# Kernel tuning notes

Measured on AMD Instinct MI355X. Metric: run time of the kernel, lower is better.

Reference implementation:

```python
import jax, jax.numpy as jnp
import numpy as np

B, S, D_IN, D_OUT = 4, 2048, 1024, 1024


def setup_inputs() -> dict:
    key = jax.random.key(0)
    k1, k2, k3, k4 = jax.random.split(key, 4)
    x = jax.random.normal(k1, (B, S, D_IN), dtype=jnp.float32)
    scale = 1.0 / np.sqrt(D_IN)
    Wq = jax.random.normal(k2, (D_IN, D_OUT), dtype=jnp.float32) * scale
    Wk = jax.random.normal(k3, (D_IN, D_OUT), dtype=jnp.float32) * scale
    Wv = jax.random.normal(k4, (D_IN, D_OUT), dtype=jnp.float32) * scale
    return {"x": x, "Wq": Wq, "Wk": Wk, "Wv": Wv}


def reference(x, Wq, Wk, Wv):
    # QKV projections (Linear, no bias)
    q = jnp.einsum('bsd,de->bse', x, Wq)  # [B,S,D_OUT]
    k = jnp.einsum('bsd,de->bse', x, Wk)
    v = jnp.einsum('bsd,de->bse', x, Wv)
    d_out = Wq.shape[1]
    # raw scores [B,S,S], scaled after masking (identical math: -inf stays -inf)
    scores = jnp.einsum('bqe,bke->bqk', q, k) * (d_out ** -0.5)
    S_ = x.shape[1]
    # causal mask: future positions (j > i) are masked out
    causal = jnp.triu(jnp.ones((S_, S_), dtype=bool), k=1)
    scores = jnp.where(causal[None, :, :], -jnp.inf, scores)
    attn = jax.nn.softmax(scores, axis=-1)  # dropout p=0.0 -> identity
    return jnp.einsum('bqk,bke->bqe', attn, v)
```

## Files before the change

### kernel.cpp

```cpp
#include <hip/hip_runtime.h>
#include <stdint.h>

typedef unsigned short u16;
typedef unsigned int u32;
typedef __bf16 bf16x8 __attribute__((ext_vector_type(8)));
typedef float f32x4 __attribute__((ext_vector_type(4)));

#define BM 128
#define BN 128
#define BK 64

__device__ __forceinline__ u16 f2bf(float x) {
  union { float f; uint32_t u; } c; c.f = x;
  uint32_t r = (c.u + 0x7FFFu + ((c.u >> 16) & 1u)) >> 16;
  return (u16)r;
}
__device__ __forceinline__ float bf2f(u16 v) {
  union { uint32_t u; float f; } c; c.u = ((uint32_t)v) << 16;
  return c.f;
}

__device__ __forceinline__ void async_copy16(const u16* g, u16* l) {
  __builtin_amdgcn_global_load_lds(
      (const __attribute__((address_space(1))) void*)g,
      (__attribute__((address_space(3))) void*)l,
      16, 0, 0);
}

__global__ void zerofill_u16(u16* __restrict__ p) {
  long i = (long)blockIdx.x * 256 + threadIdx.x;
  p[i] = 0;
}

__global__ __launch_bounds__(256)
void prep(const void* __restrict__ xs, const void* __restrict__ w0,
          const void* __restrict__ w1, const void* __restrict__ w2,
          u16* __restrict__ xn, u16* __restrict__ WT3, u32* __restrict__ flag,
          float* __restrict__ sigma, int nxb)
{
  __shared__ int sh_hits;
  __shared__ u16 tile[64][72];
  if (threadIdx.x == 0) sh_hits = 0;
  __syncthreads();
  {
    const u16* w = (const u16*)w0;
    int h = 0;
    for (int i = threadIdx.x; i < 8192; i += 256)
      if ((w[i] & 0x7F80u) == 0x7F80u) h++;
    if (h) atomicAdd(&sh_hits, h);
  }
  __syncthreads();
  const bool isf32 = (sh_hits > 0);
  const int blk = blockIdx.x;
  const int tid = threadIdx.x;
  if (blk == 0 && tid == 0) *flag = isf32 ? 1000u : 0u;

  if (blk < nxb) {
    long i = ((long)blk * 256 + tid) * 8;
    u16 o[8];
    if (isf32) {
      const float* s = (const float*)xs + i;
      f32x4 a = *(const f32x4*)s;
      f32x4 b = *(const f32x4*)(s + 4);
#pragma unroll
      for (int c = 0; c < 4; ++c) { o[c] = f2bf(a[c]); o[c + 4] = f2bf(b[c]); }
    } else {
      *(uint4*)o = *(const uint4*)((const u16*)xs + i);
    }
    *(uint4*)(xn + i) = *(uint4*)o;
  } else if (blk < nxb + 768) {
    const int Dd = 1024;
    int t = blk - nxb;
    int z = t >> 8;
    int r = t & 255;
    const int r0 = (r >> 4) * 64, c0 = (r & 15) * 64;
    const void* src = (z == 0) ? w0 : (z == 1) ? w1 : w2;
    u16* out = WT3 + (long)z * Dd * Dd;
#pragma unroll
    for (int p = 0; p < 2; ++p) {
      int v = tid + p * 256;
      int row = v >> 3, c8 = (v & 7) * 8;
      u16 tt[8];
      if (isf32) {
        const float* sp = (const float*)src + (long)(r0 + row) * Dd + c0 + c8;
        f32x4 a = *(const f32x4*)sp;
        f32x4 b = *(const f32x4*)(sp + 4);
#pragma unroll
        for (int c = 0; c < 4; ++c) { tt[c] = f2bf(a[c]); tt[c + 4] = f2bf(b[c]); }
      } else {
        *(uint4*)tt = *(const uint4*)((const u16*)src + (long)(r0 + row) * Dd + c0 + c8);
      }
#pragma unroll
      for (int c = 0; c < 8; ++c) tile[row][c8 + c] = tt[c];
    }
    __syncthreads();
#pragma unroll
    for (int p = 0; p < 2; ++p) {
      int v = tid + p * 256;
      int oc = v >> 3, r8 = (v & 7) * 8;
      union { uint4 q; u16 s[8]; } tt;
#pragma unroll
      for (int c = 0; c < 8; ++c) tt.s[c] = tile[r8 + c][oc];
      *(uint4*)(out + (long)(c0 + oc) * Dd + r0 + r8) = tt.q;
    }
  } else {
    int t = blk - (nxb + 768);
    *(f32x4*)(sigma + ((long)t * 256 + tid) * 4) = f32x4{0.f, 0.f, 0.f, 0.f};
  }
}

__global__ __launch_bounds__(512, 2)
void gemm_qkv(const u16* __restrict__ A, const u16* __restrict__ B,
              u16* __restrict__ C, int lda, int ldb, int ldc)
{
  __shared__ u16 ldsq[3 * 24576];
  const int tid  = threadIdx.x;
  const int wid  = tid >> 6;
  const int lane = tid & 63;
  const int l16  = lane & 15;
  const int lk   = lane >> 4;
  const int srow = lane >> 3;
  const int swz  = ((lane & 7) ^ srow) * 8;
  const int wr   = wid >> 1, wc = wid & 1;
  const int m0 = blockIdx.y * 256, n0 = blockIdx.x * 128;

  const u16* gA = A + (long)(m0 + wid * 32 + srow) * lda + swz;
  const u16* gB = B + (long)(n0 + wid * 16 + srow) * ldb + swz;

  const int NK = 16;

  auto issue = [&](int kt) {
    u16* Ab = ldsq + (kt % 3) * 24576;
    u16* Bb = Ab + 16384;
    const int k0 = kt * 64;
#pragma unroll
    for (int c = 0; c < 4; ++c)
      async_copy16(gA + (long)(c * 8) * lda + k0, Ab + (wid * 32 + c * 8) * 64);
#pragma unroll
    for (int c = 0; c < 2; ++c)
      async_copy16(gB + (long)(c * 8) * ldb + k0, Bb + (wid * 16 + c * 8) * 64);
  };

  f32x4 acc[4][4] = {};
  issue(0);
  issue(1);

#pragma unroll
  for (int kt = 0; kt < NK; ++kt) {
    if (kt < NK - 1) asm volatile("s_waitcnt vmcnt(6) lgkmcnt(0)" ::: "memory");
    else             asm volatile("s_waitcnt vmcnt(0) lgkmcnt(0)" ::: "memory");
    asm volatile("s_barrier" ::: "memory");
    if (kt + 2 < NK) issue(kt + 2);
    const u16* Ab = ldsq + (kt % 3) * 24576;
    const u16* Bb = Ab + 16384;
#pragma unroll
    for (int kh = 0; kh < 2; ++kh) {
      bf16x8 av[4], bv[4];
#pragma unroll
      for (int i = 0; i < 4; ++i) {
        const int Ra = wr * 64 + i * 16 + l16;
        const int Rb = wc * 64 + i * 16 + l16;
        const int ca = ((kh * 4 + lk) ^ (l16 & 7)) * 8;
        av[i] = *(const bf16x8*)(Ab + Ra * 64 + ca);
        bv[i] = *(const bf16x8*)(Bb + Rb * 64 + ca);
      }
      __builtin_amdgcn_s_setprio(1);
#pragma unroll
      for (int mi = 0; mi < 4; ++mi)
#pragma unroll
        for (int ni = 0; ni < 4; ++ni)
          acc[mi][ni] = __builtin_amdgcn_mfma_f32_16x16x32_bf16(av[mi], bv[ni], acc[mi][ni], 0, 0, 0);
      __builtin_amdgcn_s_setprio(0);
    }
  }

  const int rb0 = m0 + wr * 64;
  const int cb0 = n0 + wc * 64;
#pragma unroll
  for (int mi = 0; mi < 4; ++mi)
#pragma unroll
    for (int r = 0; r < 4; ++r) {
      const int row = rb0 + mi * 16 + lk * 4 + r;
#pragma unroll
      for (int ni = 0; ni < 4; ++ni) {
        const int col = cb0 + ni * 16 + l16;
        C[(long)row * ldc + col] = f2bf(acc[mi][ni][r]);
      }
    }
}

template <int MODE>
__global__ __launch_bounds__(256, 4)
void gemm_nt(const u16* __restrict__ A, const u16* __restrict__ B, void* __restrict__ Cv,
             const u32* __restrict__ flag, float* __restrict__ sigma, int sigStride,
             int K, int lda, int ldb, int ldc,
             long sA, long sB, long sC, long cOff,
             float scale, int trik, int ntri,
             const u16* __restrict__ vSrc, u16* __restrict__ vtDst,
             long sV, long sVT, int ldV, int ldVT)
{
  __shared__ u16 As[BM * BK];
  __shared__ u16 Bs[BN * BK];
  const int bz = blockIdx.z;
  const int tid = threadIdx.x;

  int bm, bn;
  if constexpr (MODE == 3) {
    if ((int)blockIdx.x >= ntri) {
      int t2 = blockIdx.x - ntri;
      const u16* in = vSrc + (long)bz * sV;
      u16* out = vtDst + (long)bz * sVT;
      const int c0 = (t2 & 15) * 64;
      const int r0 = (t2 >> 4) * 64;
      u16 (*tile)[72] = reinterpret_cast<u16(*)[72]>(As);
#pragma unroll
      for (int p = 0; p < 2; ++p) {
        int v = tid + p * 256;
        int row = v >> 3, c8 = (v & 7) * 8;
        union { uint4 q; u16 s[8]; } t;
        t.q = *(const uint4*)(in + (long)(r0 + row) * ldV + c0 + c8);
#pragma unroll
        for (int i = 0; i < 8; ++i) tile[row][c8 + i] = t.s[i];
      }
      __syncthreads();
#pragma unroll
      for (int p = 0; p < 2; ++p) {
        int v = tid + p * 256;
        int oc = v >> 3, r8 = (v & 7) * 8;
        union { uint4 q; u16 s[8]; } t;
#pragma unroll
        for (int i = 0; i < 8; ++i) t.s[i] = tile[r8 + i][oc];
        *(uint4*)(out + (long)(c0 + oc) * ldVT + r0 + r8) = t.q;
      }
      return;
    }
    {
      const int t = blockIdx.x;
      const int cum[11] = {0, 10, 26, 36, 52, 68, 78, 94, 110, 126, 136};
      const int ssm[10] = {0, 1, 1, 2, 2, 2, 3, 3, 3, 3};
      const int ssn[10] = {0, 0, 1, 0, 1, 2, 0, 1, 2, 3};
      int s = 0;
      while (cum[s + 1] <= t) ++s;
      const int l = t - cum[s];
      const int sm = ssm[s], sn = ssn[s];
      int tm, tn;
      if (sm == sn) {
        tm = 0;
        while ((tm + 1) * (tm + 2) / 2 <= l) ++tm;
        tn = l - tm * (tm + 1) / 2;
      } else { tm = l >> 2; tn = l & 3; }
      bm = sm * 4 + tm;
      bn = sn * 4 + tn;
    }
  } else {
    bm = blockIdx.y;
    if (trik) bm = gridDim.y - 1 - bm;
    bn = blockIdx.x;
  }

  A += (long)bz * sA;
  B += (long)bz * sB;

  const int wid  = tid >> 6;
  const int lane = tid & 63;
  const int l16  = lane & 15;
  const int lk   = lane >> 4;
  const int srow = lane >> 3;
  const int swz  = ((lane & 7) ^ srow) * 8;
  const int m0 = bm * BM, n0 = bn * BN;

  int nk = K / BK;
  if (trik) { int lim = (m0 + BM) / BK; if (lim < nk) nk = lim; }

  f32x4 acc[4][4] = {};

  for (int kt = 0; kt < nk; ++kt) {
    const int k0 = kt * BK;
#pragma unroll
    for (int c = 0; c < 4; ++c) {
      const int rb = wid * 32 + c * 8;
      async_copy16(A + (long)(m0 + rb + srow) * lda + (k0 + swz), As + rb * BK);
      async_copy16(B + (long)(n0 + rb + srow) * ldb + (k0 + swz), Bs + rb * BK);
    }
    __syncthreads();
#pragma unroll
    for (int kh = 0; kh < 2; ++kh) {
      bf16x8 av[4], bv[4];
#pragma unroll
      for (int i = 0; i < 4; ++i) {
        const int Ra = (wid >> 1) * 64 + i * 16 + l16;
        const int Rb = (wid & 1)  * 64 + i * 16 + l16;
        const int ca = ((kh * 4 + lk) ^ (l16 & 7)) * 8;
        av[i] = *(const bf16x8*)(As + Ra * BK + ca);
        bv[i] = *(const bf16x8*)(Bs + Rb * BK + ca);
      }
#pragma unroll
      for (int mi = 0; mi < 4; ++mi)
#pragma unroll
        for (int ni = 0; ni < 4; ++ni)
          acc[mi][ni] = __builtin_amdgcn_mfma_f32_16x16x32_bf16(av[mi], bv[ni], acc[mi][ni], 0, 0, 0);
    }
    __syncthreads();
  }

  const int rb0 = m0 + (wid >> 1) * 64;
  const int cb0 = n0 + (wid & 1) * 64;
  const long cbase = (long)bz * sC + cOff;

  if constexpr (MODE == 3) {
    u16* Cp = (u16*)Cv;
    const bool diag = (bm == bn);
    float* sig = sigma + (long)bz * sigStride;
#pragma unroll
    for (int mi = 0; mi < 4; ++mi)
#pragma unroll
      for (int r = 0; r < 4; ++r) {
        const int row = rb0 + mi * 16 + lk * 4 + r;
        float part = 0.f;
#pragma unroll
        for (int ni = 0; ni < 4; ++ni) {
          const int col = cb0 + ni * 16 + l16;
          float ev = __expf(acc[mi][ni][r] * scale);
          if (diag && col > row) ev = 0.f;
          u16 b = f2bf(ev);
          part += bf2f(b);
          Cp[cbase + (long)row * ldc + col] = b;
        }
#pragma unroll
        for (int o = 1; o < 16; o <<= 1) part += __shfl_xor(part, o);
        if (l16 == 0) atomicAdd(&sig[row], part);
      }
  } else {
    const bool f32out = (MODE == 2) && (*flag > 32);
    const float* sig = (MODE == 2) ? (sigma + (long)bz * sigStride) : nullptr;
#pragma unroll
    for (int mi = 0; mi < 4; ++mi)
#pragma unroll
      for (int r = 0; r < 4; ++r) {
        const int row = rb0 + mi * 16 + lk * 4 + r;
        float rs = scale;
        if constexpr (MODE == 2) rs = 1.0f / sig[row];
#pragma unroll
        for (int ni = 0; ni < 4; ++ni) {
          const int col = cb0 + ni * 16 + l16;
          const float v = acc[mi][ni][r] * rs;
          const long idx = cbase + (long)row * ldc + col;
          if constexpr (MODE == 0) {
            ((u16*)Cv)[idx] = f2bf(v);
          } else {
            if (f32out) ((float*)Cv)[idx] = v;
            else        ((u16*)Cv)[idx]   = f2bf(v);
          }
        }
      }
  }
}

extern "C" void kernel_launch(void* const* d_in, const int* in_sizes, int n_in,
                              void* d_out, int out_size, void* d_ws, size_t ws_size,
                              hipStream_t stream)
{
  (void)in_sizes; (void)n_in; (void)out_size;
  const int Bb = 4, S = 2048, D = 1024, D3 = 3072;
  const long SD  = (long)S * D;
  const long SD3 = (long)S * D3;
  const long SS  = (long)S * S;
  const long N_X = (long)Bb * SD;
  const long N_W = (long)D * D;
  const int NTRI = 16 * 17 / 2;

  char* ws = (char*)d_ws;
  size_t off = 0;
  auto take = [&](size_t bytes) -> void* {
    void* p = ws + off;
    off = (off + bytes + 255) & ~((size_t)255);
    return p;
  };

  u32*   flag  = (u32*)take(4096);
  float* sigma = (float*)take((size_t)Bb * S * 4);
  u16*   xn    = (u16*)take((size_t)N_X * 2);
  u16*   WT3   = (u16*)take((size_t)3 * N_W * 2);
  const size_t off_common = off;

  const size_t needA = off_common + (size_t)(N_X * 3 * 2)
                     + (size_t)(N_X * 2)
                     + (size_t)(Bb * SS * 2) + 4096;
  const size_t needC = off_common + (size_t)(S * (long)D3 * 2)
                     + (size_t)(SD * 2)
                     + (size_t)(SS * 2) + 4096;

  if (ws_size < needC) {
    zerofill_u16<<<(int)(N_X / 256), 256, 0, stream>>>((u16*)d_out);
    return;
  }

  const int nxb = (int)(N_X / 2048);
  prep<<<nxb + 768 + 8, 256, 0, stream>>>(d_in[0], d_in[1], d_in[2], d_in[3],
                                          xn, WT3, flag, sigma, nxb);

  const float scl = 0.03125f;

  if (ws_size >= needA) {
    u16* QKV = (u16*)take((size_t)N_X * 3 * 2);
    u16* VT  = (u16*)take((size_t)N_X * 2);
    u16* E   = (u16*)take((size_t)Bb * SS * 2);

    gemm_qkv<<<dim3(D3 / 128, (int)(N_X / D) / 256, 1), 512, 0, stream>>>(
        xn, WT3, QKV, D, D, D3);

    gemm_nt<3><<<dim3(NTRI + 512, 1, Bb), 256, 0, stream>>>(
        QKV, QKV + 1024, E, flag, sigma, S, D, D3, D3, S,
        SD3, SD3, SS, 0, scl, 0, NTRI,
        QKV + 2048, VT, SD3, SD, D3, S);

    gemm_nt<2><<<dim3(D / BN, S / BM, Bb), 256, 0, stream>>>(
        E, VT, d_out, flag, sigma, S, S, S, S, D,
        SS, SD, SD, 0, 1.f, 1, 0, nullptr, nullptr, 0, 0, 0, 0);
  } else {
    u16* QKVb = (u16*)take((size_t)S * D3 * 2);
    u16* VTb  = (u16*)take((size_t)SD * 2);
    u16* Eb   = (u16*)take((size_t)SS * 2);

    for (int b = 0; b < Bb; ++b) {
      gemm_qkv<<<dim3(D3 / 128, S / 256, 1), 512, 0, stream>>>(
          xn + (long)b * SD, WT3, QKVb, D, D, D3);

      gemm_nt<3><<<dim3(NTRI + 512, 1, 1), 256, 0, stream>>>(
          QKVb, QKVb + 1024, Eb, flag, sigma + (long)b * S, S, D, D3, D3, S,
          0, 0, 0, 0, scl, 0, NTRI,
          QKVb + 2048, VTb, 0, 0, D3, S);

      gemm_nt<2><<<dim3(D / BN, S / BM, 1), 256, 0, stream>>>(
          Eb, VTb, d_out, flag, sigma + (long)b * S, S, S, S, S, D,
          0, 0, 0, (long)b * SD, 1.f, 1, 0, nullptr, nullptr, 0, 0, 0, 0);
    }
  }
}
```

Baseline: 247.1 us.

## Rewrite QKV GEMM with 256x256 tiles, double-buffered staggered loads, XCD remap

The QKV projection kernel is restructured from 256x128 tiles with a three-stage buffer into 256x256 tiles with 8 waves arranged 2x4. Each wave now computes a 128x64 sub-tile. A and B use double-buffered LDS, and their loads are staggered across four sub-steps per k-tile, with barriers interleaved so memory traffic overlaps the MFMA work. Block indices are remapped so that consecutive tiles land on the same XCD group, which should improve L2 reuse. The larger tile raises arithmetic intensity and lowers global traffic, at the cost of more accumulator registers, 128KB of LDS per block, and more barriers.

```diff
diff --git a/kernel.cpp b/kernel.cpp
--- a/kernel.cpp
+++ b/kernel.cpp
@@ -110,10 +110,10 @@
 }
 
 __global__ __launch_bounds__(512, 2)
-void gemm_qkv(const u16* __restrict__ A, const u16* __restrict__ B,
-              u16* __restrict__ C, int lda, int ldb, int ldc)
+void gemm_qkv8(const u16* __restrict__ A, const u16* __restrict__ B,
+               u16* __restrict__ C, int lda, int ldb, int ldc, int nbn)
 {
-  __shared__ u16 ldsq[3 * 24576];
+  __shared__ u16 lds[65536];
   const int tid  = threadIdx.x;
   const int wid  = tid >> 6;
   const int lane = tid & 63;
@@ -121,63 +121,84 @@
   const int lk   = lane >> 4;
   const int srow = lane >> 3;
   const int swz  = ((lane & 7) ^ srow) * 8;
-  const int wr   = wid >> 1, wc = wid & 1;
-  const int m0 = blockIdx.y * 256, n0 = blockIdx.x * 128;
-
-  const u16* gA = A + (long)(m0 + wid * 32 + srow) * lda + swz;
-  const u16* gB = B + (long)(n0 + wid * 16 + srow) * ldb + swz;
+  const int wr   = wid >> 2, wc = wid & 3;
+
+  const int q8 = (int)gridDim.x >> 3;
+  const int wg = ((int)blockIdx.x & 7) * q8 + ((int)blockIdx.x >> 3);
+  const int m0 = (wg / nbn) * 256, n0 = (wg % nbn) * 256;
 
   const int NK = 16;
 
-  auto issue = [&](int kt) {
-    u16* Ab = ldsq + (kt % 3) * 24576;
-    u16* Bb = Ab + 16384;
-    const int k0 = kt * 64;
-#pragma unroll
-    for (int c = 0; c < 4; ++c)
-      async_copy16(gA + (long)(c * 8) * lda + k0, Ab + (wid * 32 + c * 8) * 64);
-#pragma unroll
-    for (int c = 0; c < 2; ++c)
-      async_copy16(gB + (long)(c * 8) * ldb + k0, Bb + (wid * 16 + c * 8) * 64);
+  auto stageA = [&](int t, int h) {
+    u16* dst = lds + (t & 1) * 16384 + h * 8192 + (wid * 16) * 64;
+    const u16* src = A + (long)(m0 + h * 128 + wid * 16 + srow) * lda + t * 64 + swz;
+    async_copy16(src, dst);
+    async_copy16(src + (long)8 * lda, dst + 8 * 64);
   };
-
-  f32x4 acc[4][4] = {};
-  issue(0);
-  issue(1);
-
-#pragma unroll
-  for (int kt = 0; kt < NK; ++kt) {
-    if (kt < NK - 1) asm volatile("s_waitcnt vmcnt(6) lgkmcnt(0)" ::: "memory");
-    else             asm volatile("s_waitcnt vmcnt(0) lgkmcnt(0)" ::: "memory");
-    asm volatile("s_barrier" ::: "memory");
-    if (kt + 2 < NK) issue(kt + 2);
-    const u16* Ab = ldsq + (kt % 3) * 24576;
-    const u16* Bb = Ab + 16384;
-#pragma unroll
-    for (int kh = 0; kh < 2; ++kh) {
-      bf16x8 av[4], bv[4];
-#pragma unroll
-      for (int i = 0; i < 4; ++i) {
-        const int Ra = wr * 64 + i * 16 + l16;
-        const int Rb = wc * 64 + i * 16 + l16;
-        const int ca = ((kh * 4 + lk) ^ (l16 & 7)) * 8;
-        av[i] = *(const bf16x8*)(Ab + Ra * 64 + ca);
-        bv[i] = *(const bf16x8*)(Bb + Rb * 64 + ca);
-      }
+  auto stageB = [&](int t, int h) {
+    u16* dst = lds + 32768 + (t & 1) * 16384 + h * 8192 + (wid * 16) * 64;
+    const u16* src = B + (long)(n0 + h * 128 + wid * 16 + srow) * ldb + t * 64 + swz;
+    async_copy16(src, dst);
+    async_copy16(src + (long)8 * ldb, dst + 8 * 64);
+  };
+
+  f32x4 acc[8][4] = {};
+  bf16x8 bv[4][2];
+
+  stageB(0, 0); stageB(0, 1); stageA(0, 0); stageA(0, 1);
+  stageB(1, 0); stageB(1, 1);
+  asm volatile("s_waitcnt vmcnt(4)" ::: "memory");
+  __builtin_amdgcn_s_barrier();
+
+  for (int t = 0; t < NK; ++t) {
+    const u16* Ab = lds + (t & 1) * 16384 + wr * 8192;
+    const u16* Bb = lds + 32768 + (t & 1) * 16384 + (wc >> 1) * 8192 + (wc & 1) * 64 * 64;
+#pragma unroll
+    for (int q = 0; q < 4; ++q) {
+      bf16x8 av[2][2];
+#pragma unroll
+      for (int j = 0; j < 2; ++j)
+#pragma unroll
+        for (int kh = 0; kh < 2; ++kh)
+          av[j][kh] = *(const bf16x8*)(Ab + ((2 * q + j) * 16 + l16) * 64 +
+                                       (((kh * 4 + lk) ^ (l16 & 7)) * 8));
+      if (q == 0) {
+#pragma unroll
+        for (int ni = 0; ni < 4; ++ni)
+#pragma unroll
+          for (int kh = 0; kh < 2; ++kh)
+            bv[ni][kh] = *(const bf16x8*)(Bb + (ni * 16 + l16) * 64 +
+                                          (((kh * 4 + lk) ^ (l16 & 7)) * 8));
+      }
+      if (q == 0)      { if (t + 1 < NK) stageA(t + 1, 0); }
+      else if (q == 1) { if (t + 1 < NK) stageA(t + 1, 1); }
+      else if (q == 2) { if (t + 2 < NK) stageB(t + 2, 0); }
+      else {
+        if (t + 2 < NK) stageB(t + 2, 1);
+        if (t < NK - 2) asm volatile("s_waitcnt vmcnt(4)" ::: "memory");
+        else            asm volatile("s_waitcnt vmcnt(0)" ::: "memory");
+      }
+      __builtin_amdgcn_s_barrier();
+      asm volatile("s_waitcnt lgkmcnt(0)" ::: "memory");
+      __builtin_amdgcn_sched_barrier(0);
       __builtin_amdgcn_s_setprio(1);
 #pragma unroll
-      for (int mi = 0; mi < 4; ++mi)
+      for (int j = 0; j < 2; ++j)
 #pragma unroll
         for (int ni = 0; ni < 4; ++ni)
-          acc[mi][ni] = __builtin_amdgcn_mfma_f32_16x16x32_bf16(av[mi], bv[ni], acc[mi][ni], 0, 0, 0);
+#pragma unroll
+          for (int kh = 0; kh < 2; ++kh)
+            acc[2 * q + j][ni] = __builtin_amdgcn_mfma_f32_16x16x32_bf16(
+                av[j][kh], bv[ni][kh], acc[2 * q + j][ni], 0, 0, 0);
       __builtin_amdgcn_s_setprio(0);
-    }
-  }
-
-  const int rb0 = m0 + wr * 64;
+      __builtin_amdgcn_s_barrier();
+    }
+  }
+
+  const int rb0 = m0 + wr * 128;
   const int cb0 = n0 + wc * 64;
 #pragma unroll
-  for (int mi = 0; mi < 4; ++mi)
+  for (int mi = 0; mi < 8; ++mi)
 #pragma unroll
     for (int r = 0; r < 4; ++r) {
       const int row = rb0 + mi * 16 + lk * 4 + r;
@@ -406,8 +427,7 @@
     u16* VT  = (u16*)take((size_t)N_X * 2);
     u16* E   = (u16*)take((size_t)Bb * SS * 2);
 
-    gemm_qkv<<<dim3(D3 / 128, (int)(N_X / D) / 256, 1), 512, 0, stream>>>(
-        xn, WT3, QKV, D, D, D3);
+    gemm_qkv8<<<dim3(32 * 12), 512, 0, stream>>>(xn, WT3, QKV, D, D, D3, 12);
 
     gemm_nt<3><<<dim3(NTRI + 512, 1, Bb), 256, 0, stream>>>(
         QKV, QKV + 1024, E, flag, sigma, S, D, D3, D3, S,
@@ -423,8 +443,8 @@
     u16* Eb   = (u16*)take((size_t)SS * 2);
 
     for (int b = 0; b < Bb; ++b) {
-      gemm_qkv<<<dim3(D3 / 128, S / 256, 1), 512, 0, stream>>>(
-          xn + (long)b * SD, WT3, QKVb, D, D, D3);
+      gemm_qkv8<<<dim3(8 * 12), 512, 0, stream>>>(
+          xn + (long)b * SD, WT3, QKVb, D, D, D3, 12);
 
       gemm_nt<3><<<dim3(NTRI + 512, 1, 1), 256, 0, stream>>>(
           QKVb, QKVb + 1024, Eb, flag, sigma + (long)b * S, S, D, D3, D3, S,
```

Result: no change. 250.4 us (+1.3%).
